# Performance work log

Hardware: AMD Instinct MI355X
Metric: run time of the kernel (lower is better)

## Reference

```python
import jax, jax.numpy as jnp
import numpy as np

TEMPERATURE = 0.1
NEGATIVE_WEIGHT = 1.0
NORM_EPS = 1e-12  # matches torch F.normalize clamp_min eps


def setup_inputs() -> dict:
    key = jax.random.key(0)
    x = jax.random.normal(key, (8, 128, 16, 8, 8), dtype=jnp.float32)
    return {"x": x}


def reference(x):
    B, F, T, H, W = x.shape
    # transpose(0,1).flatten(1).transpose(0,1): (B,F,T,H,W) -> (N, F), N = B*T*H*W
    feats = jnp.transpose(x, (1, 0, 2, 3, 4)).reshape(F, -1).T  # [N, F]
    norms = jnp.maximum(jnp.linalg.norm(feats, axis=1, keepdims=True), NORM_EPS)
    x_norm = feats / norms  # unit vectors, [N, F]
    sims = (x_norm @ x_norm.T) / TEMPERATURE  # [N, N] cosine similarities
    n = sims.shape[0]
    # masked_select(~eye) + logsumexp == logsumexp with diagonal set to -inf
    sims = jnp.where(jnp.eye(n, dtype=bool), -jnp.inf, sims)
    diversity_loss = jax.nn.logsumexp(sims)
    return NEGATIVE_WEIGHT * diversity_loss
```

## Files before the change

kernel.cpp:

```cpp
#include <hip/hip_runtime.h>
#include <hip/hip_fp8.h>
#include <math.h>


#define NTILE 8256
#define NPBLK 1536

typedef __attribute__((ext_vector_type(4))) float f32x4;

__device__ inline unsigned char f2fp8(float f) {
    __hip_fp8_e4m3 h(f);
    return h.__x;
}

__global__ __launch_bounds__(256)
void normalize_kernel(const float* __restrict__ x, unsigned char* __restrict__ Xs) {
    __shared__ float ldsf[128][33];
    __shared__ float ssred[8][32];
    __shared__ float invs[32];
    const int tid = threadIdx.x;
    const int b  = blockIdx.x >> 5;
    const int r0 = (blockIdx.x & 31) * 32;
    const int rl = tid & 31, fp = tid >> 5;
    const float* px = x + b * 131072 + r0 + rl;
    float ss = 0.f;
#pragma unroll
    for (int j = 0; j < 16; ++j) {
        int f = fp * 16 + j;
        float v = px[f * 1024];
        ldsf[f][rl] = v;
        ss = fmaf(v, v, ss);
    }
    ssred[fp][rl] = ss;
    __syncthreads();
    if (tid < 32) {
        float s = 0.f;
#pragma unroll
        for (int k = 0; k < 8; ++k) s += ssred[k][tid];
        invs[tid] = 1.0f / fmaxf(sqrtf(s), 1e-12f);
    }
    __syncthreads();
    {
        const int c   = tid;
        const int rgl = c >> 7;
        const int cc  = c & 127;
        const int t8  = (cc >> 6) & 1, q = (cc >> 4) & 3, r = cc & 15;
        const int row = rgl * 16 + r;
        const float inv = invs[row];
        union { unsigned char bytes[16]; int4 v; } u;
#pragma unroll
        for (int half = 0; half < 2; ++half)
#pragma unroll
            for (int j = 0; j < 8; ++j) {
                int k = t8 * 64 + half * 32 + q * 8 + j;
                u.bytes[half * 8 + j] = f2fp8(ldsf[k][row] * inv);
            }
        const int rgg = blockIdx.x * 2 + rgl;
        ((int4*)Xs)[rgg * 128 + cc] = u.v;
    }
}

__global__ __launch_bounds__(256, 6)
void gram_lse_kernel(const int4* __restrict__ Xs, float* __restrict__ partials) {
    const int bk = blockIdx.x;
    const int tid = threadIdx.x;
    const int lane = tid & 63, w = tid >> 6;
    const int ga = (w & 1) * 2;
    const int gb = (w >> 1) * 2;
    const int quad = lane >> 4, colL = lane & 15;
    const float C = 14.426950408889634f;
    float wsum = 0.f;

    for (int tile = bk; tile < NTILE; tile += NPBLK) {
        int L = tile, I = 0;
        while (L >= 128 - I) { L -= 128 - I; ++I; }
        const int J = I + L;

        const int argb = I * 4 + ga;
        const int brgb = J * 4 + gb;
        int4 av[2][2], bv[2][2];
#pragma unroll
        for (int g = 0; g < 2; ++g)
#pragma unroll
            for (int t8 = 0; t8 < 2; ++t8) {
                av[g][t8] = Xs[(argb + g) * 128 + t8 * 64 + lane];
                bv[g][t8] = Xs[(brgb + g) * 128 + t8 * 64 + lane];
            }

        f32x4 acc[2][2];
#pragma unroll
        for (int i = 0; i < 2; ++i)
#pragma unroll
            for (int j = 0; j < 2; ++j) acc[i][j] = (f32x4){0.f, 0.f, 0.f, 0.f};

#pragma unroll
        for (int t = 0; t < 4; ++t) {
            long aL[2], bL[2];
#pragma unroll
            for (int g = 0; g < 2; ++g) {
                aL[g] = ((const long*)&av[g][t >> 1])[t & 1];
                bL[g] = ((const long*)&bv[g][t >> 1])[t & 1];
            }
#pragma unroll
            for (int i = 0; i < 2; ++i)
#pragma unroll
                for (int j = 0; j < 2; ++j)
                    acc[i][j] = __builtin_amdgcn_mfma_f32_16x16x32_fp8_fp8(
                        aL[i], bL[j], acc[i][j], 0, 0, 0);
        }

        const bool diagT = (I == J);
        float lsum = 0.f;
#pragma unroll
        for (int i = 0; i < 2; ++i) {
            const int rbase = (ga + i) * 16 + quad * 4;
#pragma unroll
            for (int j = 0; j < 2; ++j) {
                const int cbase = (gb + j) * 16 + colL;
#pragma unroll
                for (int g = 0; g < 4; ++g) {
                    if (diagT && (rbase + g == cbase)) continue;
                    lsum += exp2f(fmaf(C, acc[i][j][g], -C));
                }
            }
        }
        wsum += diagT ? lsum : 2.0f * lsum;
    }

#pragma unroll
    for (int o = 32; o > 0; o >>= 1) wsum += __shfl_down(wsum, o, 64);
    __shared__ float red[4];
    if (lane == 0) red[w] = wsum;
    __syncthreads();
    if (tid == 0) partials[bk] = red[0] + red[1] + red[2] + red[3];
}

__global__ __launch_bounds__(256)
void final_kernel(const float* __restrict__ partials, float* __restrict__ out) {
    double s = 0.0;
    for (int i = threadIdx.x; i < NPBLK; i += 256) s += (double)partials[i];
#pragma unroll
    for (int o = 32; o > 0; o >>= 1) s += __shfl_down(s, o, 64);
    __shared__ double red[4];
    if ((threadIdx.x & 63) == 0) red[threadIdx.x >> 6] = s;
    __syncthreads();
    if (threadIdx.x == 0)
        out[0] = (float)(10.0 + log(red[0] + red[1] + red[2] + red[3]));
}

extern "C" void kernel_launch(void* const* d_in, const int* in_sizes, int n_in,
                              void* d_out, int out_size, void* d_ws, size_t ws_size,
                              hipStream_t stream) {
    const float* x = (const float*)d_in[0];
    float* out = (float*)d_out;
    float* partials = (float*)d_ws;
    unsigned char* Xs = (unsigned char*)d_ws + 131072;

    normalize_kernel<<<256, 256, 0, stream>>>(x, Xs);
    gram_lse_kernel<<<NPBLK, 256, 0, stream>>>((const int4*)Xs, partials);
    final_kernel<<<1, 256, 0, stream>>>(partials, out);
}
```

Before: 81.59 us.

## Assign contiguous tile runs per block, reuse A fragments, use fast exp2 and packed fp8

Each gram block now handles six consecutive upper-triangular tiles, 1376*6 = NTILE, instead of a strided set. The row-tile index is computed once rather than per tile, and A-operand loads are skipped when the row tile stays the same. The exp2 call becomes the hardware builtin, and fp8 conversion in normalize uses packed cvt instructions. The cost is a fully unrolled fixed loop with conditional reloads and fewer blocks launched.

```diff
diff --git a/kernel.cpp b/kernel.cpp
--- a/kernel.cpp
+++ b/kernel.cpp
@@ -4,13 +4,28 @@
 
 
 #define NTILE 8256
-#define NPBLK 1536
+#define NPBLK 1376
 
 typedef __attribute__((ext_vector_type(4))) float f32x4;
 
-__device__ inline unsigned char f2fp8(float f) {
-    __hip_fp8_e4m3 h(f);
-    return h.__x;
+#if __has_builtin(__builtin_amdgcn_exp2f)
+#define EXP2F(x) __builtin_amdgcn_exp2f(x)
+#else
+#define EXP2F(x) exp2f(x)
+#endif
+
+__device__ inline unsigned int pk_fp8(float f0, float f1, float f2, float f3) {
+#if __has_builtin(__builtin_amdgcn_cvt_pk_fp8_f32)
+    unsigned int r = 0;
+    r = __builtin_amdgcn_cvt_pk_fp8_f32(f0, f1, r, false);
+    r = __builtin_amdgcn_cvt_pk_fp8_f32(f2, f3, r, true);
+    return r;
+#else
+    union { unsigned char b[4]; unsigned int u; } v;
+    v.b[0] = __hip_fp8_e4m3(f0).__x; v.b[1] = __hip_fp8_e4m3(f1).__x;
+    v.b[2] = __hip_fp8_e4m3(f2).__x; v.b[3] = __hip_fp8_e4m3(f3).__x;
+    return v.u;
+#endif
 }
 
 __global__ __launch_bounds__(256)
@@ -47,14 +62,15 @@
         const int t8  = (cc >> 6) & 1, q = (cc >> 4) & 3, r = cc & 15;
         const int row = rgl * 16 + r;
         const float inv = invs[row];
-        union { unsigned char bytes[16]; int4 v; } u;
+        union { unsigned int w[4]; int4 v; } u;
 #pragma unroll
-        for (int half = 0; half < 2; ++half)
-#pragma unroll
-            for (int j = 0; j < 8; ++j) {
-                int k = t8 * 64 + half * 32 + q * 8 + j;
-                u.bytes[half * 8 + j] = f2fp8(ldsf[k][row] * inv);
-            }
+        for (int half = 0; half < 2; ++half) {
+            const int k0 = t8 * 64 + half * 32 + q * 8;
+            u.w[half * 2 + 0] = pk_fp8(ldsf[k0 + 0][row] * inv, ldsf[k0 + 1][row] * inv,
+                                       ldsf[k0 + 2][row] * inv, ldsf[k0 + 3][row] * inv);
+            u.w[half * 2 + 1] = pk_fp8(ldsf[k0 + 4][row] * inv, ldsf[k0 + 5][row] * inv,
+                                       ldsf[k0 + 6][row] * inv, ldsf[k0 + 7][row] * inv);
+        }
         const int rgg = blockIdx.x * 2 + rgl;
         ((int4*)Xs)[rgg * 128 + cc] = u.v;
     }
@@ -69,30 +85,38 @@
     const int gb = (w >> 1) * 2;
     const int quad = lane >> 4, colL = lane & 15;
     const float C = 14.426950408889634f;
+
+    int L = bk * 6, I = 0;
+    while (L >= 128 - I) { L -= 128 - I; ++I; }
+    int J = I + L;
+
     float wsum = 0.f;
-
-    for (int tile = bk; tile < NTILE; tile += NPBLK) {
-        int L = tile, I = 0;
-        while (L >= 128 - I) { L -= 128 - I; ++I; }
-        const int J = I + L;
-
-        const int argb = I * 4 + ga;
+    int Icur = -1;
+    int4 av[2][2];
+#pragma unroll
+    for (int s = 0; s < 6; ++s) {
+        if (I != Icur) {
+            const int argb = I * 4 + ga;
+#pragma unroll
+            for (int g = 0; g < 2; ++g)
+#pragma unroll
+                for (int t8 = 0; t8 < 2; ++t8)
+                    av[g][t8] = Xs[(argb + g) * 128 + t8 * 64 + lane];
+            Icur = I;
+        }
         const int brgb = J * 4 + gb;
-        int4 av[2][2], bv[2][2];
+        int4 bv[2][2];
 #pragma unroll
         for (int g = 0; g < 2; ++g)
 #pragma unroll
-            for (int t8 = 0; t8 < 2; ++t8) {
-                av[g][t8] = Xs[(argb + g) * 128 + t8 * 64 + lane];
+            for (int t8 = 0; t8 < 2; ++t8)
                 bv[g][t8] = Xs[(brgb + g) * 128 + t8 * 64 + lane];
-            }
 
         f32x4 acc[2][2];
 #pragma unroll
         for (int i = 0; i < 2; ++i)
 #pragma unroll
             for (int j = 0; j < 2; ++j) acc[i][j] = (f32x4){0.f, 0.f, 0.f, 0.f};
-
 #pragma unroll
         for (int t = 0; t < 4; ++t) {
             long aL[2], bL[2];
@@ -120,11 +144,13 @@
 #pragma unroll
                 for (int g = 0; g < 4; ++g) {
                     if (diagT && (rbase + g == cbase)) continue;
-                    lsum += exp2f(fmaf(C, acc[i][j][g], -C));
+                    lsum += EXP2F(fmaf(C, acc[i][j][g], -C));
                 }
             }
         }
         wsum += diagT ? lsum : 2.0f * lsum;
+
+        if (++J == 128) { ++I; J = I; }
     }
 
 #pragma unroll
```

New measurement: 87.18 us. +6.9%, slower.
